# Performance work log

Measured on AMD Instinct MI355X. Metric: run time of the kernel, lower is better.

The kernel has to match this reference:

```python
import jax, jax.numpy as jnp
import numpy as np

P = 128  # fixed patch width (coord[3k] == 128 for all k)


def setup_inputs() -> dict:
    key = jax.random.key(0)
    B, C, H, W = 32, 3, 512, 512
    inputs = jax.random.normal(key, (B, C, H, W), dtype=jnp.float32)
    j = np.arange(B)
    # (i1, i2) offsets matching the coord list in init_kwargs
    starts = jnp.asarray(
        np.stack([(37 * j) % (H - P), (53 * j) % (W - P)], axis=1),
        dtype=jnp.int32,
    )
    return {"inputs": inputs, "starts": starts}


def reference(inputs, starts):
    # inputs: [B, C, H, W] float32; starts: [B, 2] int32 (i1, i2 per image)
    B, C, H, W = inputs.shape

    def crop_resize(img, st):
        # crop PxP patch, then bilinear-upsample back to (H, W)
        patch = jax.lax.dynamic_slice(img, (0, st[0], st[1]), (C, P, P))
        # half-pixel-center bilinear == torch bilinear align_corners=False
        # (antialias is a no-op when upsampling)
        return jax.image.resize(patch, (C, H, W), method="bilinear")

    return jax.vmap(crop_resize)(inputs, starts)  # [B, C, H, W]
```

## Files before the change

kernel.cpp:

```cpp
#include <hip/hip_runtime.h>


#define PP   128
#define HH   512
#define WW   512
#define CC   3

__global__ __launch_bounds__(256) void crop_resize4x_kernel(
    const float* __restrict__ in,
    const int*   __restrict__ starts,
    float*       __restrict__ out,
    int total_groups)
{
    const int stride = gridDim.x * blockDim.x;
    for (int t = blockIdx.x * blockDim.x + threadIdx.x; t < total_groups; t += stride) {
        const int qx = t & 127;
        const int y  = (t >> 7) & 511;
        const int bc = t >> 16;
        const int b  = bc / 3;

        const int s0 = starts[2 * b];
        const int s1 = starts[2 * b + 1];
        const float* patch = in + ((size_t)bc * HH + s0) * WW + s1;

        const int qy = y >> 2;
        const int ry = y & 3;
        int y0, y1;
        float w1;
        if (ry < 2) { y0 = qy - 1; y1 = qy;     w1 = (ry == 0) ? 0.625f : 0.875f; }
        else        { y0 = qy;     y1 = qy + 1; w1 = (ry == 2) ? 0.125f : 0.375f; }
        const float w0 = 1.0f - w1;
        y0 = max(y0, 0);
        y1 = min(y1, PP - 1);
        const float* r0 = patch + (size_t)y0 * WW;
        const float* r1 = patch + (size_t)y1 * WW;

        const int xa = max(qx - 1, 0);
        const int xb = qx;
        const int xc = min(qx + 1, PP - 1);

        const float va = w0 * r0[xa] + w1 * r1[xa];
        const float vb = w0 * r0[xb] + w1 * r1[xb];
        const float vc = w0 * r0[xc] + w1 * r1[xc];

        float4 o;
        o.x = 0.375f * va + 0.625f * vb;
        o.y = 0.125f * va + 0.875f * vb;
        o.z = 0.875f * vb + 0.125f * vc;
        o.w = 0.625f * vb + 0.375f * vc;

        const size_t oidx = ((size_t)bc * HH + y) * WW + ((size_t)qx << 2);
        *reinterpret_cast<float4*>(out + oidx) = o;
    }
}

extern "C" void kernel_launch(void* const* d_in, const int* in_sizes, int n_in,
                              void* d_out, int out_size, void* d_ws, size_t ws_size,
                              hipStream_t stream) {
    const float* in     = (const float*)d_in[0];
    const int*   starts = (const int*)d_in[1];
    float*       out    = (float*)d_out;

    const int B = in_sizes[1] / 2;
    const int total_groups = B * CC * HH * (WW / 4);

    const int block = 256;
    int grid = (total_groups + block - 1) / block;
    if (grid > 2048) grid = 2048;

    crop_resize4x_kernel<<<grid, block, 0, stream>>>(in, starts, out, total_groups);
}
```

Before: 26.59 us.

## Compute 4x4 output block per thread with nontemporal stores

Each thread now loads a 3x3 input neighbourhood and writes a full 4x4 output block (four float4 rows), instead of one float4 per thread with a 2x3 load. This cuts redundant input loads and index math per output, and removes the grid-stride loop in favour of one thread per block. The stores use nontemporal hints so the write-only output streams past the cache. Each wavefront's stores are now spread across four rows, which could reduce write coalescing.

```diff
diff --git a/kernel.cpp b/kernel.cpp
--- a/kernel.cpp
+++ b/kernel.cpp
@@ -6,51 +6,60 @@
 #define WW   512
 #define CC   3
 
-__global__ __launch_bounds__(256) void crop_resize4x_kernel(
+typedef float f32x4 __attribute__((ext_vector_type(4)));
+
+__global__ __launch_bounds__(256) void crop_resize4x_blk_kernel(
     const float* __restrict__ in,
     const int*   __restrict__ starts,
-    float*       __restrict__ out,
-    int total_groups)
+    float*       __restrict__ out)
 {
-    const int stride = gridDim.x * blockDim.x;
-    for (int t = blockIdx.x * blockDim.x + threadIdx.x; t < total_groups; t += stride) {
-        const int qx = t & 127;
-        const int y  = (t >> 7) & 511;
-        const int bc = t >> 16;
-        const int b  = bc / 3;
+    const int t  = blockIdx.x * blockDim.x + threadIdx.x;
+    const int qx = t & 127;
+    const int qy = (t >> 7) & 127;
+    const int bc = t >> 14;
+    const int b  = bc / 3;
 
-        const int s0 = starts[2 * b];
-        const int s1 = starts[2 * b + 1];
-        const float* patch = in + ((size_t)bc * HH + s0) * WW + s1;
+    const int s0 = starts[2 * b];
+    const int s1 = starts[2 * b + 1];
+    const float* patch = in + ((size_t)bc * HH + s0) * WW + s1;
 
-        const int qy = y >> 2;
-        const int ry = y & 3;
-        int y0, y1;
-        float w1;
-        if (ry < 2) { y0 = qy - 1; y1 = qy;     w1 = (ry == 0) ? 0.625f : 0.875f; }
-        else        { y0 = qy;     y1 = qy + 1; w1 = (ry == 2) ? 0.125f : 0.375f; }
-        const float w0 = 1.0f - w1;
-        y0 = max(y0, 0);
-        y1 = min(y1, PP - 1);
-        const float* r0 = patch + (size_t)y0 * WW;
-        const float* r1 = patch + (size_t)y1 * WW;
+    const int ya = max(qy - 1, 0);
+    const int yc = min(qy + 1, PP - 1);
+    const int xa = max(qx - 1, 0);
+    const int xc = min(qx + 1, PP - 1);
 
-        const int xa = max(qx - 1, 0);
-        const int xb = qx;
-        const int xc = min(qx + 1, PP - 1);
+    const float* rA = patch + (size_t)ya * WW;
+    const float* rB = patch + (size_t)qy * WW;
+    const float* rC = patch + (size_t)yc * WW;
 
-        const float va = w0 * r0[xa] + w1 * r1[xa];
-        const float vb = w0 * r0[xb] + w1 * r1[xb];
-        const float vc = w0 * r0[xc] + w1 * r1[xc];
+    const float aA = rA[xa], aB = rA[qx], aC = rA[xc];
+    const float bA = rB[xa], bB = rB[qx], bC = rB[xc];
+    const float cA = rC[xa], cB = rC[qx], cC = rC[xc];
 
-        float4 o;
-        o.x = 0.375f * va + 0.625f * vb;
-        o.y = 0.125f * va + 0.875f * vb;
-        o.z = 0.875f * vb + 0.125f * vc;
-        o.w = 0.625f * vb + 0.375f * vc;
+    float vA[4], vB[4], vC[4];
+    vA[0] = 0.375f * aA + 0.625f * bA;
+    vB[0] = 0.375f * aB + 0.625f * bB;
+    vC[0] = 0.375f * aC + 0.625f * bC;
+    vA[1] = 0.125f * aA + 0.875f * bA;
+    vB[1] = 0.125f * aB + 0.875f * bB;
+    vC[1] = 0.125f * aC + 0.875f * bC;
+    vA[2] = 0.875f * bA + 0.125f * cA;
+    vB[2] = 0.875f * bB + 0.125f * cB;
+    vC[2] = 0.875f * bC + 0.125f * cC;
+    vA[3] = 0.625f * bA + 0.375f * cA;
+    vB[3] = 0.625f * bB + 0.375f * cB;
+    vC[3] = 0.625f * bC + 0.375f * cC;
 
-        const size_t oidx = ((size_t)bc * HH + y) * WW + ((size_t)qx << 2);
-        *reinterpret_cast<float4*>(out + oidx) = o;
+    float* orow = out + ((size_t)bc * HH + ((size_t)qy << 2)) * WW + ((size_t)qx << 2);
+
+    #pragma unroll
+    for (int ry = 0; ry < 4; ++ry) {
+        f32x4 o;
+        o.x = 0.375f * vA[ry] + 0.625f * vB[ry];
+        o.y = 0.125f * vA[ry] + 0.875f * vB[ry];
+        o.z = 0.875f * vB[ry] + 0.125f * vC[ry];
+        o.w = 0.625f * vB[ry] + 0.375f * vC[ry];
+        __builtin_nontemporal_store(o, reinterpret_cast<f32x4*>(orow + (size_t)ry * WW));
     }
 }
 
@@ -62,11 +71,9 @@
     float*       out    = (float*)d_out;
 
     const int B = in_sizes[1] / 2;
-    const int total_groups = B * CC * HH * (WW / 4);
+    const int total_threads = B * CC * PP * PP;
+    const int block = 256;
+    const int grid = (total_threads + block - 1) / block;
 
-    const int block = 256;
-    int grid = (total_groups + block - 1) / block;
-    if (grid > 2048) grid = 2048;
-
-    crop_resize4x_kernel<<<grid, block, 0, stream>>>(in, starts, out, total_groups);
+    crop_resize4x_blk_kernel<<<grid, block, 0, stream>>>(in, starts, out);
 }
```

Measured after the change: 21.56 us. 1.23x faster.
